# Kernel optimization log

Measured on AMD Instinct MI355X. Metric: run time of the kernel, lower is better.

## Reference

```python
import jax, jax.numpy as jnp
import numpy as np

B, T, J, V, D, H = 32, 400, 30, 50000, 150, 150
L = 2  # answer_token_len (boundary model: start, end)


def _gru_step(h, x, Wih, Whh, bih, bhh):
    # torch GRUCell semantics
    gi = x @ Wih.T + bih
    gh = h @ Whh.T + bhh
    ir, iz, inn = jnp.split(gi, 3, axis=-1)
    hr, hz, hn = jnp.split(gh, 3, axis=-1)
    r = jax.nn.sigmoid(ir + hr)
    z = jax.nn.sigmoid(iz + hz)
    n = jnp.tanh(inn + r * hn)
    return (1.0 - z) * n + z * h


def _gru_seq(x, Wih, Whh, bih, bhh):
    # x: [B, S, din] -> hidden sequence [B, S, h]
    h0 = jnp.zeros((x.shape[0], Whh.shape[1]), x.dtype)
    def step(h, xt):
        h = _gru_step(h, xt, Wih, Whh, bih, bhh)
        return h, h
    _, hs = jax.lax.scan(step, h0, jnp.swapaxes(x, 0, 1))
    return jnp.swapaxes(hs, 0, 1)


def _forward(context, query,
             E,
             ctx_Wih, ctx_Whh, ctx_bih, ctx_bhh,
             q_Wih, q_Whh, q_bih, q_bhh,
             Wq, Wp, Wr, w, gate_bias, attn_bias,
             m_Wih, m_Whh, m_bih, m_bhh,
             mr_Wih, mr_Whh, mr_bih, mr_bhh,
             ptr_W1, ptr_W2, ptr_v,
             d_Wih, d_Whh, d_bih, d_bhh):
    # encode context and query with GRUs
    Hp = _gru_seq(E[context], ctx_Wih, ctx_Whh, ctx_bih, ctx_bhh)  # [B,T,H]
    Hq = _gru_seq(E[query], q_Wih, q_Whh, q_bih, q_bhh)            # [B,J,H]

    whq = jnp.einsum('bjh,hk->bjk', Hq, Wq)  # precomputed query projection [B,J,H]

    def match_scan(xs, cWih, cWhh, cbih, cbhh):
        # xs: [B,T,H] context encodings (possibly time-reversed)
        def step(h, xt):
            # G_i = tanh(Wq Hq + (Wp p_i + Wr h_{i-1}) + bias)  -> [B,J,H]
            g = jnp.tanh(whq + (xt @ Wp + h @ Wr + gate_bias)[:, None, :])
            a = jax.nn.softmax(g @ w + attn_bias, axis=-1)       # [B,J]
            q = jnp.einsum('bj,bjh->bh', a, Hq)                  # attended query
            z = jnp.concatenate([xt, q], axis=-1)                # [B,2H]
            h = _gru_step(h, z, cWih, cWhh, cbih, cbhh)
            return h, h
        h0 = jnp.zeros((xs.shape[0], xs.shape[2]), xs.dtype)
        _, hs = jax.lax.scan(step, h0, jnp.swapaxes(xs, 0, 1))
        return jnp.swapaxes(hs, 0, 1)  # [B,T,H]

    Hf = match_scan(Hp, m_Wih, m_Whh, m_bih, m_bhh)              # forward direction
    Hb = match_scan(Hp[:, ::-1], mr_Wih, mr_Whh, mr_bih, mr_bhh) # reverse direction (scan order, as original)
    Hr = jnp.concatenate([Hf, Hb], axis=-1)                      # [B,T,2H]
    zero0 = jnp.zeros((Hr.shape[0], 1, Hr.shape[2]), Hr.dtype)   # initial zero state prepended
    Hr = jnp.concatenate([zero0, Hr], axis=1)                    # [B,T+1,2H]

    # boundary pointer network: L attention steps over H_r
    enc = Hr @ ptr_W1
    def ptr_step(h, _):
        s = jnp.tanh(enc + (h @ ptr_W2)[:, None, :]) @ ptr_v     # [B,T+1]
        a = jax.nn.softmax(s, axis=-1)
        c = jnp.einsum('bt,bth->bh', a, Hr)
        h = _gru_step(h, c, d_Wih, d_Whh, d_bih, d_bhh)
        return h, a
    h0 = jnp.zeros((Hr.shape[0], Hr.shape[2]), Hr.dtype)
    _, probs = jax.lax.scan(ptr_step, h0, None, length=L)
    return jnp.swapaxes(probs, 0, 1)  # [B, L, T+1]


def setup_inputs() -> dict:
    key = jax.random.key(0)
    keys = iter(jax.random.split(key, 40))
    p = lambda *s: jax.random.normal(next(keys), s, jnp.float32) * 0.05
    inp = {
        'context': jax.random.randint(next(keys), (B, T), 0, V, dtype=jnp.int32),
        'query': jax.random.randint(next(keys), (B, J), 0, V, dtype=jnp.int32),
        'E': p(V, D),
        'ctx_Wih': p(3 * H, D), 'ctx_Whh': p(3 * H, H), 'ctx_bih': p(3 * H), 'ctx_bhh': p(3 * H),
        'q_Wih': p(3 * H, D), 'q_Whh': p(3 * H, H), 'q_bih': p(3 * H), 'q_bhh': p(3 * H),
        'Wq': p(H, H), 'Wp': p(H, H), 'Wr': p(H, H), 'w': p(H),
        'gate_bias': p(H), 'attn_bias': p(),
        'm_Wih': p(3 * H, 2 * H), 'm_Whh': p(3 * H, H), 'm_bih': p(3 * H), 'm_bhh': p(3 * H),
        'mr_Wih': p(3 * H, 2 * H), 'mr_Whh': p(3 * H, H), 'mr_bih': p(3 * H), 'mr_bhh': p(3 * H),
        'ptr_W1': p(2 * H, 2 * H), 'ptr_W2': p(2 * H, 2 * H), 'ptr_v': p(2 * H),
        'd_Wih': p(6 * H, 2 * H), 'd_Whh': p(6 * H, 2 * H), 'd_bih': p(6 * H), 'd_bhh': p(6 * H),
    }
    return inp


def reference(context, query, E,
              ctx_Wih, ctx_Whh, ctx_bih, ctx_bhh,
              q_Wih, q_Whh, q_bih, q_bhh,
              Wq, Wp, Wr, w, gate_bias, attn_bias,
              m_Wih, m_Whh, m_bih, m_bhh,
              mr_Wih, mr_Whh, mr_bih, mr_bhh,
              ptr_W1, ptr_W2, ptr_v,
              d_Wih, d_Whh, d_bih, d_bhh):
    return _forward(context, query, E,
                    ctx_Wih, ctx_Whh, ctx_bih, ctx_bhh,
                    q_Wih, q_Whh, q_bih, q_bhh,
                    Wq, Wp, Wr, w, gate_bias, attn_bias,
                    m_Wih, m_Whh, m_bih, m_bhh,
                    mr_Wih, mr_Whh, mr_bih, mr_bhh,
                    ptr_W1, ptr_W2, ptr_v,
                    d_Wih, d_Whh, d_bih, d_bhh)
```

## Files before the change

### kernel.cpp

```cpp
#include <hip/hip_runtime.h>
#include <hip/hip_bf16.h>


namespace {

constexpr int NBATCH = 32;
constexpr int TLEN   = 400;
constexpr int JQ     = 30;
constexpr int T1     = 401;

__device__ __forceinline__ float sigm(float x){ return 1.f/(1.f+__expf(-x)); }
__device__ __forceinline__ float tanh_f(float x){
  float e = __expf(-2.f*fabsf(x));
  float t = (1.f-e)/(1.f+e);
  return x < 0.f ? -t : t;
}
__device__ __forceinline__ float bf2f(unsigned short u){
  union { unsigned int i; float f; } c; c.i = ((unsigned int)u)<<16; return c.f;
}

__device__ __forceinline__ void bar_lds(){
  asm volatile("s_waitcnt lgkmcnt(0)" ::: "memory");
  __builtin_amdgcn_s_barrier();
}

#define NW 29
struct WDesc { const void* src[NW]; int off[NW+1]; };

__global__ void sniff_kernel(const unsigned int* __restrict__ bits, int* __restrict__ flag){
  __shared__ int cnt;
  if (threadIdx.x==0) cnt = 0;
  __syncthreads();
  int hit = 0;
  #pragma unroll
  for (int i=0;i<4;i++){
    unsigned int w = bits[threadIdx.x*4+i];
    unsigned int b = (w>>8)&0x7Fu;
    if (b==0u || (b>=0x38u && b<=0x3Fu)) hit++;
  }
  atomicAdd(&cnt, hit);
  __syncthreads();
  if (threadIdx.x==0) *flag = (cnt > 768) ? 1 : 0;
}

__global__ void convert_weights_kernel(WDesc d, float* __restrict__ out, const int* __restrict__ flag){
  const int isbf = *flag;
  const int total = d.off[NW];
  for (int e = blockIdx.x*blockDim.x+threadIdx.x; e < total; e += gridDim.x*blockDim.x){
    int j = 0;
    while (e >= d.off[j+1]) j++;
    int i = e - d.off[j];
    out[e] = isbf ? bf2f(((const unsigned short*)d.src[j])[i])
                  : ((const float*)d.src[j])[i];
  }
}

__global__ void padrows_kernel(const float* __restrict__ src, float* __restrict__ dst,
                               int rows, int cols, int ldd){
  int i = blockIdx.x*blockDim.x+threadIdx.x;
  if (i >= rows*ldd) return;
  int r = i/ldd, c = i-r*ldd;
  dst[i] = (c<cols) ? src[(size_t)r*cols+c] : 0.f;
}

__global__ void transpose_kernel(const float* __restrict__ src, float* __restrict__ dst,
                                 int R, int C, int lds_, int offs){
  int idx = blockIdx.x*blockDim.x+threadIdx.x;
  if (idx >= R*C) return;
  int i = idx / R, k = idx - i*R;
  dst[(size_t)i*R + k] = src[(size_t)k*lds_ + offs + i];
}

__global__ void build_wcat_kernel(const float* __restrict__ Whh, const float* __restrict__ Wr,
                                  float* __restrict__ Wcat){
  int i = blockIdx.x*blockDim.x+threadIdx.x;
  if (i >= 600*152) return;
  int r = i/152, c = i-r*152;
  float v = 0.f;
  if (c < 150){
    if (r < 450) v = Whh[(size_t)r*150+c];
    else         v = Wr[(size_t)c*150 + (r-450)];
  }
  Wcat[i] = v;
}

__global__ void build_msplit_kernel(const float* __restrict__ Wcat,
                                    float* __restrict__ s2q, float* __restrict__ ext){
  int i = blockIdx.x*blockDim.x+threadIdx.x;
  if (i < 24576){
    int q = i/2048, rem = i-q*2048, r = rem/4, p = rem-r*4;
    s2q[i] = Wcat[(size_t)r*152 + 104 + 4*q + p];
  } else if (i < 24576+13376){
    int k = i-24576;
    int q = k/352, rem = k-q*352, ii = rem/4, p = rem-ii*4;
    ext[k] = Wcat[(size_t)(512+ii)*152 + 4*q + p];
  }
}

__global__ void build_gsplit_kernel(const float* __restrict__ Wpad, float* __restrict__ s2q){
  int i = blockIdx.x*blockDim.x+threadIdx.x;
  if (i >= 12*452*4) return;
  int q = i/1808, rem = i-q*1808, r = rem/4, p = rem-r*4;
  s2q[i] = (r<450) ? Wpad[(size_t)r*152 + 104 + 4*q + p] : 0.f;
}

__global__ __launch_bounds__(512) void rowproj16_kernel(
    const float* __restrict__ Xrows,
    const int* __restrict__ gather, const void* __restrict__ Etab, const int* __restrict__ bfflag,
    const float* __restrict__ W, const float* __restrict__ bias,
    float* __restrict__ out, int rows, int K, int inner, int ldw, int ldo)
{
  __shared__ __align__(16) float xs[16][304];
  const int r0 = blockIdx.x*16;
  int nr = rows - r0; if (nr > 16) nr = 16;
  if (nr <= 0) return;
  const int isbf = gather ? *bfflag : 0;
  for (int e = threadIdx.x; e < nr*inner; e += 512){
    int r = e/inner, i = e - r*inner;
    float v;
    if (gather){
      size_t base = (size_t)gather[r0+r]*inner + i;
      v = isbf ? bf2f(((const unsigned short*)Etab)[base]) : ((const float*)Etab)[base];
    } else {
      v = Xrows[(size_t)(r0+r)*inner + i];
    }
    xs[r][i] = v;
  }
  __syncthreads();
  for (int k = threadIdx.x; k < K; k += 512){
    float b0 = bias ? bias[k] : 0.f;
    float acc[16];
    #pragma unroll
    for (int r=0;r<16;r++) acc[r] = b0;
    int i = 0;
    for (; i+4 <= inner; i += 4){
      float w0 = W[(size_t)i*ldw + k];
      float w1 = W[(size_t)(i+1)*ldw + k];
      float w2 = W[(size_t)(i+2)*ldw + k];
      float w3 = W[(size_t)(i+3)*ldw + k];
      #pragma unroll
      for (int r=0;r<16;r++){
        float4 xv = *(const float4*)&xs[r][i];
        acc[r] = fmaf(xv.x, w0, acc[r]);
        acc[r] = fmaf(xv.y, w1, acc[r]);
        acc[r] = fmaf(xv.z, w2, acc[r]);
        acc[r] = fmaf(xv.w, w3, acc[r]);
      }
    }
    for (; i < inner; i++){
      float wv = W[(size_t)i*ldw + k];
      #pragma unroll
      for (int r=0;r<16;r++) acc[r] = fmaf(xs[r][i], wv, acc[r]);
    }
    for (int r=0;r<nr;r++) out[(size_t)(r0+r)*ldo + k] = acc[r];
  }
  for (int k = K + threadIdx.x; k < ldo; k += 512)
    for (int r=0;r<nr;r++) out[(size_t)(r0+r)*ldo + k] = 0.f;
}

#define R26(M) M(0) M(1) M(2) M(3) M(4) M(5) M(6) M(7) M(8) M(9) M(10) M(11) \
               M(12) M(13) M(14) M(15) M(16) M(17) M(18) M(19) M(20) M(21) \
               M(22) M(23) M(24) M(25)
#define R12(M) M(26) M(27) M(28) M(29) M(30) M(31) M(32) M(33) M(34) M(35) \
               M(36) M(37)
#define DECW(i) float4 w##i;
#define LDW(i)  w##i = wrow4[i];
#define LDW2(i) w##i = s2q4[(i-26)*s2stride + s2r];
#define FMAW(i) { float4 hq = h4[i]; \
  acc0 = fmaf(hq.x, w##i.x, acc0); acc1 = fmaf(hq.y, w##i.y, acc1); \
  acc2 = fmaf(hq.z, w##i.z, acc2); acc3 = fmaf(hq.w, w##i.w, acc3); }

__global__ __launch_bounds__(512, 2) void gru_scan_kernel(
    const float* __restrict__ gi0, const float* __restrict__ Wp0,
    const float* __restrict__ s2q0, const float* __restrict__ bh0,
    float* __restrict__ H0, int S0,
    const float* __restrict__ gi1, const float* __restrict__ Wp1,
    const float* __restrict__ s2q1, const float* __restrict__ bh1,
    float* __restrict__ H1, int S1)
{
  const int blk = blockIdx.x;
  const float* gi; const float* Wpad; const float* s2qG; const float* bh; float* Hs; int S;
  if (blk < 32){ gi = gi0 + (size_t)blk*S0*450;  Wpad = Wp0; s2qG = s2q0; bh = bh0;
                 Hs = H0 + (size_t)blk*S0*150;   S = S0; }
  else         { int bb = blk-32;
                 gi = gi1 + (size_t)bb*S1*450;   Wpad = Wp1; s2qG = s2q1; bh = bh1;
                 Hs = H1 + (size_t)bb*S1*150;    S = S1; }
  __shared__ __align__(16) float h[152];
  __shared__ float gh[452];
  const int tid = threadIdx.x;

  R26(DECW) R12(DECW)
  float br = 0.f;
  {
    const float4* wrow4 = (const float4*)(Wpad + (size_t)((tid<450)?tid:0)*152);
    R26(LDW)
    const float4* s2q4 = (const float4*)s2qG;
    const int s2stride = 452; const int s2r = (tid<452) ? tid : 0;
    R12(LDW2)
    if (tid<450) br = bh[tid];
  }
  if (tid < 152) h[tid] = 0.f;
  __syncthreads();
  const float4* h4 = (const float4*)h;

  for (int t=0;t<S;t++){
    float g0=0.f,g1=0.f,g2=0.f;
    if (tid < 150){
      const float* gg = gi + (size_t)t*450;
      g0 = gg[tid]; g1 = gg[150+tid]; g2 = gg[300+tid];
    }
    if (tid < 450){
      float acc0=br, acc1=0.f, acc2=0.f, acc3=0.f;
      R26(FMAW) R12(FMAW)
      gh[tid] = (acc0+acc2)+(acc1+acc3);
    }
    bar_lds();
    if (tid < 150){
      float r = sigm(g0 + gh[tid]);
      float z = sigm(g1 + gh[150+tid]);
      float n = tanh_f(g2 + r*gh[300+tid]);
      float hn = (1.f-z)*n + z*h[tid];
      h[tid] = hn;
      Hs[(size_t)t*150 + tid] = hn;
    }
    bar_lds();
  }
}

__global__ void zero_hr0_kernel(float* __restrict__ Hr){
  int idx = blockIdx.x*blockDim.x + threadIdx.x;
  if (idx < NBATCH*300){
    int b = idx/300, k = idx - 300*b;
    Hr[(size_t)b*T1*300 + k] = 0.f;
  }
}

__global__ __launch_bounds__(512, 2) void match_scan_kernel(
    const float* __restrict__ pWp,
    const float* __restrict__ whq,
    const float* __restrict__ giXf,
    const float* __restrict__ giXr,
    const float* __restrict__ Pf,
    const float* __restrict__ Pr,
    const float* __restrict__ WcatF, const float* __restrict__ WcatR,
    const float* __restrict__ s2qF,  const float* __restrict__ s2qR,
    const float* __restrict__ extF,  const float* __restrict__ extR,
    const float* __restrict__ m_bhh, const float* __restrict__ mr_bhh,
    const float* __restrict__ wvec,
    float* __restrict__ Hr)
{
  const int b   = blockIdx.x;
  const int dir = blockIdx.y;
  const float* giX  = dir ? giXr : giXf;
  const float* P    = dir ? Pr   : Pf;
  const float* Wcat = dir ? WcatR : WcatF;
  const float* s2qG = dir ? s2qR  : s2qF;
  const float* extG = dir ? extR  : extF;
  const float* bhh  = dir ? mr_bhh : m_bhh;

  __shared__ float4 extW[3344];
  __shared__ __align__(16) float Ps[JQ*452];
  __shared__ __align__(16) float whqS[JQ*152];
  __shared__ __align__(16) float wrP[760];
  __shared__ __align__(16) float h[152];
  __shared__ float ghsRaw[512];
  __shared__ __align__(16) float pwS[152];
  __shared__ __align__(16) float wlS[152];
  __shared__ float sc[32];

  const int tid  = threadIdx.x;
  const int lane = tid & 63;
  const int wv   = tid >> 6;
  const int er   = (tid < 440) ? (tid % 88) : 0;
  const int kg   = (tid < 440) ? (tid / 88) : 0;

  R26(DECW) R12(DECW)
  float br;
  {
    const float4* wrow4 = (const float4*)(Wcat + (size_t)tid*152);
    R26(LDW)
    const float4* s2q4 = (const float4*)s2qG;
    const int s2stride = 512; const int s2r = tid;
    R12(LDW2)
    br = (tid < 450) ? bhh[tid] : 0.f;
  }
  for (int e=tid; e<3344; e+=512) extW[e] = ((const float4*)extG)[e];
  {
    const float* Pb = P + (size_t)b*JQ*452;
    for (int e=tid; e<JQ*452; e+=512) Ps[e] = Pb[e];
    const float4* wq4 = (const float4*)(whq + (size_t)b*JQ*152);
    for (int e=tid; e<JQ*38; e+=512) ((float4*)whqS)[e] = wq4[e];
  }
  for (int e=tid; e<760; e+=512) wrP[e] = 0.f;
  if (tid < 152){
    h[tid] = 0.f;
    wlS[tid] = (tid<150) ? wvec[tid] : 0.f;
  }
  __syncthreads();
  const float4* h4 = (const float4*)h;
  const float4* wrP4 = (const float4*)wrP;

  for (int t=0;t<TLEN;t++){
    const int tt = dir ? (TLEN-1-t) : t;

    float gv0=0.f, gv1=0.f, gv2=0.f;
    if (tid < 150){
      const float* g = giX + ((size_t)b*TLEN + tt)*452;
      gv0 = g[tid]; gv1 = g[150+tid]; gv2 = g[300+tid];
    }
    float4 pwv;
    if (tid >= 440 && tid < 478)
      pwv = ((const float4*)(pWp + ((size_t)b*TLEN + tt)*152))[tid-440];

    {
      float acc0=br, acc1=0.f, acc2=0.f, acc3=0.f;
      R26(FMAW) R12(FMAW)
      float v = (acc0+acc2)+(acc1+acc3);
      ghsRaw[tid] = v;
      if (tid >= 450) wrP[tid-450] = v;
    }
    if (tid < 440){
      float e0=0.f, e1=0.f;
      #pragma unroll
      for (int j=0;j<8;j++){
        int q = kg*8+j;
        if (q < 38){
          float4 wq = extW[q*88+er]; float4 hq = h4[q];
          e0 = fmaf(hq.x,wq.x,e0); e1 = fmaf(hq.y,wq.y,e1);
          e0 = fmaf(hq.z,wq.z,e0); e1 = fmaf(hq.w,wq.w,e1);
        }
      }
      wrP[kg*152 + 62 + er] = e0+e1;
    }
    if (tid >= 440 && tid < 478) ((float4*)pwS)[tid-440] = pwv;
    bar_lds();

    {
      float4 b4; b4.x=b4.y=b4.z=b4.w=0.f;
      const bool bl = (lane < 38);
      if (bl){
        float4 pw4 = ((const float4*)pwS)[lane];
        float4 s0 = wrP4[lane],        s1 = wrP4[38+lane];
        float4 s2 = wrP4[76+lane],     s3 = wrP4[114+lane];
        float4 s4 = wrP4[152+lane];
        b4.x = pw4.x + s0.x+s1.x+s2.x+s3.x+s4.x;
        b4.y = pw4.y + s0.y+s1.y+s2.y+s3.y+s4.y;
        b4.z = pw4.z + s0.z+s1.z+s2.z+s3.z+s4.z;
        b4.w = pw4.w + s0.w+s1.w+s2.w+s3.w+s4.w;
      }
      #pragma unroll
      for (int jj=0;jj<4;jj++){
        int j = wv + 8*jj;
        float a = 0.f;
        if (j < JQ && bl){
          float4 q4 = ((const float4*)whqS)[j*38 + lane];
          float4 w4 = ((const float4*)wlS)[lane];
          a = w4.x*tanh_f(q4.x+b4.x);
          a = fmaf(w4.y, tanh_f(q4.y+b4.y), a);
          a = fmaf(w4.z, tanh_f(q4.z+b4.z), a);
          a = fmaf(w4.w, tanh_f(q4.w+b4.w), a);
        }
        #pragma unroll
        for (int off=32; off; off>>=1) a += __shfl_down(a, off);
        if (j < JQ && lane==0) sc[j] = a;
      }
    }
    bar_lds();

    if (tid < 192){
      float v = (lane < JQ) ? sc[lane] : -1e30f;
      float m = v;
      #pragma unroll
      for (int off=32; off; off>>=1) m = fmaxf(m, __shfl_down(m, off));
      m = __shfl(m, 0);
      float e = (lane < JQ) ? __expf(v-m) : 0.f;
      float su = e;
      #pragma unroll
      for (int off=32; off; off>>=1) su += __shfl_down(su, off);
      su = __shfl(su, 0);
      float aw = e/su;
      const int k = (tid < 150) ? tid : 0;
      float accr = gv0, accz = gv1, accn = gv2;
      #pragma unroll
      for (int j=0;j<JQ;j++){
        float aj = __shfl(aw, j);
        accr = fmaf(aj, Ps[j*452 + k],       accr);
        accz = fmaf(aj, Ps[j*452 + 150 + k], accz);
        accn = fmaf(aj, Ps[j*452 + 300 + k], accn);
      }
      if (tid < 150){
        float r = sigm(accr + ghsRaw[tid]);
        float z = sigm(accz + ghsRaw[150+tid]);
        float n = tanh_f(accn + r*ghsRaw[300+tid]);
        float hn = (1.f-z)*n + z*h[tid];
        h[tid] = hn;
        Hr[((size_t)b*T1 + (t+1))*300 + dir*150 + tid] = hn;
      }
    }
    bar_lds();
  }
}

__global__ __launch_bounds__(512,2) void ptr_scan_kernel(
    const float* __restrict__ enc, const float* __restrict__ Hr,
    const float* __restrict__ W2, const float* __restrict__ pv,
    const float* __restrict__ dWih, const float* __restrict__ dWhh,
    const float* __restrict__ dbih, const float* __restrict__ dbhh,
    void* __restrict__ outv, const int* __restrict__ flag)
{
  const int b = blockIdx.x;
  const int tid = threadIdx.x;
  const int isbf = *flag;
  __shared__ float h[300], hW2[300], sl[T1], al[T1], c[300];
  __shared__ float gis[900], ghs[900];
  __shared__ float vl[300];
  __shared__ float red[8];
  if (tid < 300){ h[tid] = 0.f; vl[tid] = pv[tid]; }
  __syncthreads();
  for (int l=0;l<2;l++){
    if (tid < 300){
      float a0=0.f,a1=0.f;
      for (int i=0;i<300;i+=2){
        a0 += h[i]  *W2[(size_t)i*300+tid];
        a1 += h[i+1]*W2[(size_t)(i+1)*300+tid];
      }
      hW2[tid] = a0+a1;
    }
    __syncthreads();
    {
      const int wv = tid>>6, lane = tid&63;
      for (int t=wv; t<T1; t+=8){
        const float* er = enc + ((size_t)b*T1 + t)*300;
        float acc = 0.f;
        for (int k=lane; k<300; k+=64) acc += vl[k]*tanh_f(er[k] + hW2[k]);
        #pragma unroll
        for (int off=32; off; off>>=1) acc += __shfl_down(acc, off);
        if (lane==0) sl[t] = acc;
      }
    }
    __syncthreads();
    {
      float v = (tid < T1) ? sl[tid] : -1e30f;
      float m = v;
      #pragma unroll
      for (int off=32; off; off>>=1) m = fmaxf(m, __shfl_down(m, off));
      if ((tid&63)==0) red[tid>>6] = m;
      __syncthreads();
      float bm = fmaxf(fmaxf(fmaxf(red[0],red[1]),fmaxf(red[2],red[3])),
                       fmaxf(fmaxf(red[4],red[5]),fmaxf(red[6],red[7])));
      float e = (tid < T1) ? __expf(v-bm) : 0.f;
      float su = e;
      #pragma unroll
      for (int off=32; off; off>>=1) su += __shfl_down(su, off);
      __syncthreads();
      if ((tid&63)==0) red[tid>>6] = su;
      __syncthreads();
      float bs = red[0]+red[1]+red[2]+red[3]+red[4]+red[5]+red[6]+red[7];
      if (tid < T1){
        float a = e/bs;
        al[tid] = a;
        size_t oi = ((size_t)b*2 + l)*T1 + tid;
        if (isbf) ((__hip_bfloat16*)outv)[oi] = __float2bfloat16(a);
        else      ((float*)outv)[oi] = a;
      }
    }
    __syncthreads();
    if (tid < 300){
      float acc = 0.f;
      for (int t=0;t<T1;t++) acc += al[t]*Hr[((size_t)b*T1 + t)*300 + tid];
      c[tid] = acc;
    }
    __syncthreads();
    for (int k=tid; k<900; k+=blockDim.x){
      const float* wi = dWih + (size_t)k*300;
      const float* wh = dWhh + (size_t)k*300;
      float a0 = dbih[k], a1 = dbhh[k];
      for (int i=0;i<300;i++){ a0 += c[i]*wi[i]; a1 += h[i]*wh[i]; }
      gis[k] = a0; ghs[k] = a1;
    }
    __syncthreads();
    if (tid < 300){
      float r = sigm(gis[tid] + ghs[tid]);
      float z = sigm(gis[300+tid] + ghs[300+tid]);
      float n = tanh_f(gis[600+tid] + r*ghs[600+tid]);
      h[tid] = (1.f-z)*n + z*h[tid];
    }
    __syncthreads();
  }
}

}

extern "C" void kernel_launch(void* const* d_in, const int* in_sizes, int n_in,
                              void* d_out, int out_size, void* d_ws, size_t ws_size,
                              hipStream_t stream)
{
  (void)in_sizes; (void)n_in; (void)out_size; (void)ws_size;
  float* ws = (float*)d_ws;
  int* flag = (int*)d_ws;

  static const int wsz[NW] = {
    67500,67500,450,450,
    67500,67500,450,450,
    22500,22500,22500,150,150,1,
    135000,67500,450,450,
    135000,67500,450,450,
    90000,90000,300,
    270000,270000,900,900
  };
  WDesc desc;
  int cum = 0;
  for (int j=0;j<NW;j++){ desc.src[j] = d_in[3+j]; desc.off[j] = cum; cum += wsz[j]; }
  desc.off[NW] = cum;

  float* WB = ws + 16;
  const float* P_ctx_Wih = WB + desc.off[0];
  const float* P_ctx_Whh = WB + desc.off[1];
  const float* P_ctx_bih = WB + desc.off[2];
  const float* P_ctx_bhh = WB + desc.off[3];
  const float* P_q_Wih   = WB + desc.off[4];
  const float* P_q_Whh   = WB + desc.off[5];
  const float* P_q_bih   = WB + desc.off[6];
  const float* P_q_bhh   = WB + desc.off[7];
  const float* P_Wq      = WB + desc.off[8];
  const float* P_Wp      = WB + desc.off[9];
  const float* P_Wr      = WB + desc.off[10];
  const float* P_w       = WB + desc.off[11];
  const float* P_gb      = WB + desc.off[12];
  const float* P_m_Wih   = WB + desc.off[14];
  const float* P_m_Whh   = WB + desc.off[15];
  const float* P_m_bih   = WB + desc.off[16];
  const float* P_m_bhh   = WB + desc.off[17];
  const float* P_mr_Wih  = WB + desc.off[18];
  const float* P_mr_Whh  = WB + desc.off[19];
  const float* P_mr_bih  = WB + desc.off[20];
  const float* P_mr_bhh  = WB + desc.off[21];
  const float* P_W1      = WB + desc.off[22];
  const float* P_W2      = WB + desc.off[23];
  const float* P_pv      = WB + desc.off[24];
  const float* P_dWih    = WB + desc.off[25];
  const float* P_dWhh    = WB + desc.off[26];
  const float* P_dbih    = WB + desc.off[27];
  const float* P_dbhh    = WB + desc.off[28];

  size_t p = 16 + 1468512;
  float* ctxWhhP = ws + p; p += 68400;
  float* qWhhP   = ws + p; p += 68400;
  float* s2qCtx  = ws + p; p += 21696;
  float* s2qQ    = ws + p; p += 21696;
  float* WcatF   = ws + p; p += 91200;
  float* WcatR   = ws + p; p += 91200;
  float* s2qF    = ws + p; p += 24576;
  float* s2qR    = ws + p; p += 24576;
  float* extFg   = ws + p; p += 13376;
  float* extRg   = ws + p; p += 13376;
  float* ctxWihT = ws + p; p += 67500;
  float* qWihT   = ws + p; p += 67500;
  float* mXfT    = ws + p; p += 67500;
  float* mXrT    = ws + p; p += 67500;
  float* mQfT    = ws + p; p += 67500;
  float* mQrT    = ws + p; p += 67500;

  float* ctx_gi = ws + p; p += 5760000;
  float* q_gi   = ws + p; p += 432000;
  float* HpB    = ws + p; p += 1920000;
  float* HqB    = ws + p; p += 144000;
  float* whqB   = ws + p; p += 145920;
  float* PfB    = ws + p; p += 433920;
  float* PrB    = ws + p; p += 433920;
  float* pWpB   = ws + p; p += 1945600;
  float* giXfB  = ws + p; p += 5785600;
  float* giXrB  = ws + p; p += 5785600;
  float* HrB    = ws + p; p += 3849600;
  float* encB   = ctx_gi;

  sniff_kernel<<<1,256,0,stream>>>((const unsigned int*)d_in[2], flag);
  convert_weights_kernel<<<512,256,0,stream>>>(desc, WB, flag);
  padrows_kernel<<<(450*152+255)/256,256,0,stream>>>(P_ctx_Whh, ctxWhhP, 450,150,152);
  padrows_kernel<<<(450*152+255)/256,256,0,stream>>>(P_q_Whh,   qWhhP,   450,150,152);
  build_gsplit_kernel<<<(12*452*4+255)/256,256,0,stream>>>(ctxWhhP, s2qCtx);
  build_gsplit_kernel<<<(12*452*4+255)/256,256,0,stream>>>(qWhhP,   s2qQ);
  build_wcat_kernel<<<(600*152+255)/256,256,0,stream>>>(P_m_Whh,  P_Wr, WcatF);
  build_wcat_kernel<<<(600*152+255)/256,256,0,stream>>>(P_mr_Whh, P_Wr, WcatR);
  build_msplit_kernel<<<(24576+13376+255)/256,256,0,stream>>>(WcatF, s2qF, extFg);
  build_msplit_kernel<<<(24576+13376+255)/256,256,0,stream>>>(WcatR, s2qR, extRg);
  transpose_kernel<<<(67500+255)/256,256,0,stream>>>(P_ctx_Wih, ctxWihT, 450,150,150,0);
  transpose_kernel<<<(67500+255)/256,256,0,stream>>>(P_q_Wih,   qWihT,   450,150,150,0);
  transpose_kernel<<<(67500+255)/256,256,0,stream>>>(P_m_Wih,   mXfT,    450,150,300,0);
  transpose_kernel<<<(67500+255)/256,256,0,stream>>>(P_mr_Wih,  mXrT,    450,150,300,0);
  transpose_kernel<<<(67500+255)/256,256,0,stream>>>(P_m_Wih,   mQfT,    450,150,300,150);
  transpose_kernel<<<(67500+255)/256,256,0,stream>>>(P_mr_Wih,  mQrT,    450,150,300,150);

  rowproj16_kernel<<<800,512,0,stream>>>(nullptr,(const int*)d_in[0], d_in[2], flag,
                                         ctxWihT, P_ctx_bih, ctx_gi, 12800,450,150,450,450);
  rowproj16_kernel<<<60,512,0,stream>>>(nullptr,(const int*)d_in[1], d_in[2], flag,
                                        qWihT, P_q_bih, q_gi, 960,450,150,450,450);

  gru_scan_kernel<<<64,512,0,stream>>>(ctx_gi, ctxWhhP, s2qCtx, P_ctx_bhh, HpB, 400,
                                       q_gi,   qWhhP,   s2qQ,   P_q_bhh,   HqB, 30);

  rowproj16_kernel<<<60,512,0,stream>>>(HqB,nullptr,nullptr,nullptr, P_Wq, nullptr,
                                        whqB, 960,150,150,150,152);
  rowproj16_kernel<<<60,512,0,stream>>>(HqB,nullptr,nullptr,nullptr, mQfT, nullptr,
                                        PfB, 960,450,150,450,452);
  rowproj16_kernel<<<60,512,0,stream>>>(HqB,nullptr,nullptr,nullptr, mQrT, nullptr,
                                        PrB, 960,450,150,450,452);
  rowproj16_kernel<<<800,512,0,stream>>>(HpB,nullptr,nullptr,nullptr, P_Wp, P_gb,
                                         pWpB, 12800,150,150,150,152);
  rowproj16_kernel<<<800,512,0,stream>>>(HpB,nullptr,nullptr,nullptr, mXfT, P_m_bih,
                                         giXfB, 12800,450,150,450,452);
  rowproj16_kernel<<<800,512,0,stream>>>(HpB,nullptr,nullptr,nullptr, mXrT, P_mr_bih,
                                         giXrB, 12800,450,150,450,452);

  zero_hr0_kernel<<<(NBATCH*300+511)/512,512,0,stream>>>(HrB);
  match_scan_kernel<<<dim3(NBATCH,2),512,0,stream>>>(pWpB, whqB, giXfB, giXrB,
                                                     PfB, PrB, WcatF, WcatR,
                                                     s2qF, s2qR, extFg, extRg,
                                                     P_m_bhh, P_mr_bhh, P_w, HrB);

  rowproj16_kernel<<<802,512,0,stream>>>(HrB,nullptr,nullptr,nullptr, P_W1, nullptr,
                                         encB, 12832,300,300,300,300);
  ptr_scan_kernel<<<32,512,0,stream>>>(encB, HrB, P_W2, P_pv,
                                       P_dWih, P_dWhh, P_dbih, P_dbhh, d_out, flag);
}
```

Measured before the change: 3.498 ms.

## Keep match-scan weights in registers and transpose attention projection in LDS

The extension weights and the per-batch query projection plus attention vector move from shared memory into per-thread registers, loaded once before the time loop. The P matrix is stored transposed in LDS so each thread reads contiguous float4 rows. Every softmax thread now computes the full 30-way softmax from the shared scores instead of using cross-lane shuffles. The aim is to cut LDS traffic, shuffles and serial latency inside the 400-step recurrence, at the cost of higher register pressure under 512-thread launch bounds, which could cause spills.

```diff
diff --git a/kernel.cpp b/kernel.cpp
--- a/kernel.cpp
+++ b/kernel.cpp
@@ -17,6 +17,14 @@
 }
 __device__ __forceinline__ float bf2f(unsigned short u){
   union { unsigned int i; float f; } c; c.i = ((unsigned int)u)<<16; return c.f;
+}
+__device__ __forceinline__ float q4max(float4 v){ return fmaxf(fmaxf(v.x,v.y),fmaxf(v.z,v.w)); }
+__device__ __forceinline__ float sum4(float4 v){ return (v.x+v.y)+(v.z+v.w); }
+__device__ __forceinline__ float4 exp4(float4 v, float m){
+  return make_float4(__expf(v.x-m),__expf(v.y-m),__expf(v.z-m),__expf(v.w-m));
+}
+__device__ __forceinline__ float4 scl4(float4 v, float s){
+  return make_float4(v.x*s,v.y*s,v.z*s,v.w*s);
 }
 
 __device__ __forceinline__ void bar_lds(){
@@ -163,12 +171,19 @@
                M(22) M(23) M(24) M(25)
 #define R12(M) M(26) M(27) M(28) M(29) M(30) M(31) M(32) M(33) M(34) M(35) \
                M(36) M(37)
+#define E8(M)  M(0) M(1) M(2) M(3) M(4) M(5) M(6) M(7)
 #define DECW(i) float4 w##i;
 #define LDW(i)  w##i = wrow4[i];
 #define LDW2(i) w##i = s2q4[(i-26)*s2stride + s2r];
 #define FMAW(i) { float4 hq = h4[i]; \
   acc0 = fmaf(hq.x, w##i.x, acc0); acc1 = fmaf(hq.y, w##i.y, acc1); \
   acc2 = fmaf(hq.z, w##i.z, acc2); acc3 = fmaf(hq.w, w##i.w, acc3); }
+#define DECE(j) float4 ex##j;
+#define LDE(j)  { int q = kg*8+j; \
+  ex##j = (tid<440 && q<38) ? extG4[q*88+er] : make_float4(0.f,0.f,0.f,0.f); }
+#define FMAE(j) { float4 hq = h4[kg*8+j]; \
+  f0 = fmaf(hq.x, ex##j.x, f0); f1 = fmaf(hq.y, ex##j.y, f1); \
+  f0 = fmaf(hq.z, ex##j.z, f0); f1 = fmaf(hq.w, ex##j.w, f1); }
 
 __global__ __launch_bounds__(512, 2) void gru_scan_kernel(
     const float* __restrict__ gi0, const float* __restrict__ Wp0,
@@ -258,16 +273,12 @@
   const float* extG = dir ? extR  : extF;
   const float* bhh  = dir ? mr_bhh : m_bhh;
 
-  __shared__ float4 extW[3344];
-  __shared__ __align__(16) float Ps[JQ*452];
-  __shared__ __align__(16) float whqS[JQ*152];
+  __shared__ __align__(16) float PsT[15000];
   __shared__ __align__(16) float wrP[760];
-  __shared__ __align__(16) float h[152];
+  __shared__ __align__(16) float h[160];
   __shared__ float ghsRaw[512];
   __shared__ __align__(16) float pwS[152];
-  __shared__ __align__(16) float wlS[152];
-  __shared__ float sc[32];
-
+  __shared__ __align__(16) float sc[32];
   const int tid  = threadIdx.x;
   const int lane = tid & 63;
   const int wv   = tid >> 6;
@@ -284,17 +295,35 @@
     R12(LDW2)
     br = (tid < 450) ? bhh[tid] : 0.f;
   }
-  for (int e=tid; e<3344; e+=512) extW[e] = ((const float4*)extG)[e];
+  const float4* extG4 = (const float4*)extG;
+  E8(DECE) E8(LDE)
+  const float4* wqg = (const float4*)(whq + (size_t)b*JQ*152);
+  const int ln38 = (lane < 38) ? lane : 0;
+  float4 wq0 = wqg[(size_t)(wv     )*38 + ln38];
+  float4 wq1 = wqg[(size_t)(wv +  8)*38 + ln38];
+  float4 wq2 = wqg[(size_t)(wv + 16)*38 + ln38];
+  float4 wq3 = (wv + 24 < JQ) ? wqg[(size_t)(wv + 24)*38 + ln38]
+                              : make_float4(0.f,0.f,0.f,0.f);
+  float4 wl4 = make_float4(0.f,0.f,0.f,0.f);
+  if (lane < 38){
+    wl4 = ((const float4*)wvec)[lane];
+    if (lane == 37){ wl4.z = 0.f; wl4.w = 0.f; }
+  }
+
+  for (int e=tid; e<15000; e+=512) PsT[e] = 0.f;
+  for (int e=tid; e<760;   e+=512) wrP[e] = 0.f;
+  if (tid < 160) h[tid] = 0.f;
+  if (tid >= 30 && tid < 32) sc[tid] = -1e30f;
+  __syncthreads();
   {
     const float* Pb = P + (size_t)b*JQ*452;
-    for (int e=tid; e<JQ*452; e+=512) Ps[e] = Pb[e];
-    const float4* wq4 = (const float4*)(whq + (size_t)b*JQ*152);
-    for (int e=tid; e<JQ*38; e+=512) ((float4*)whqS)[e] = wq4[e];
-  }
-  for (int e=tid; e<760; e+=512) wrP[e] = 0.f;
-  if (tid < 152){
-    h[tid] = 0.f;
-    wlS[tid] = (tid<150) ? wvec[tid] : 0.f;
+    for (int e=tid; e<JQ*452; e+=512){
+      int j = e/452, kk = e - j*452;
+      if (kk < 450){
+        int g = kk/150, k = kk - g*150;
+        PsT[k*100 + g*32 + j] = Pb[e];
+      }
+    }
   }
   __syncthreads();
   const float4* h4 = (const float4*)h;
@@ -319,24 +348,16 @@
       ghsRaw[tid] = v;
       if (tid >= 450) wrP[tid-450] = v;
     }
-    if (tid < 440){
-      float e0=0.f, e1=0.f;
-      #pragma unroll
-      for (int j=0;j<8;j++){
-        int q = kg*8+j;
-        if (q < 38){
-          float4 wq = extW[q*88+er]; float4 hq = h4[q];
-          e0 = fmaf(hq.x,wq.x,e0); e1 = fmaf(hq.y,wq.y,e1);
-          e0 = fmaf(hq.z,wq.z,e0); e1 = fmaf(hq.w,wq.w,e1);
-        }
-      }
-      wrP[kg*152 + 62 + er] = e0+e1;
+    {
+      float f0=0.f, f1=0.f;
+      E8(FMAE)
+      if (tid < 440) wrP[kg*152 + 62 + er] = f0+f1;
     }
     if (tid >= 440 && tid < 478) ((float4*)pwS)[tid-440] = pwv;
     bar_lds();
 
     {
-      float4 b4; b4.x=b4.y=b4.z=b4.w=0.f;
+      float4 b4 = make_float4(0.f,0.f,0.f,0.f);
       const bool bl = (lane < 38);
       if (bl){
         float4 pw4 = ((const float4*)pwS)[lane];
@@ -348,46 +369,45 @@
         b4.z = pw4.z + s0.z+s1.z+s2.z+s3.z+s4.z;
         b4.w = pw4.w + s0.w+s1.w+s2.w+s3.w+s4.w;
       }
-      #pragma unroll
-      for (int jj=0;jj<4;jj++){
-        int j = wv + 8*jj;
-        float a = 0.f;
-        if (j < JQ && bl){
-          float4 q4 = ((const float4*)whqS)[j*38 + lane];
-          float4 w4 = ((const float4*)wlS)[lane];
-          a = w4.x*tanh_f(q4.x+b4.x);
-          a = fmaf(w4.y, tanh_f(q4.y+b4.y), a);
-          a = fmaf(w4.z, tanh_f(q4.z+b4.z), a);
-          a = fmaf(w4.w, tanh_f(q4.w+b4.w), a);
-        }
-        #pragma unroll
-        for (int off=32; off; off>>=1) a += __shfl_down(a, off);
-        if (j < JQ && lane==0) sc[j] = a;
-      }
+      #define BSCORE(jj, WQ) { const int j = wv + 8*jj; float a = 0.f; \
+        if (j < JQ && bl){ \
+          a = wl4.x*tanh_f(WQ.x+b4.x); \
+          a = fmaf(wl4.y, tanh_f(WQ.y+b4.y), a); \
+          a = fmaf(wl4.z, tanh_f(WQ.z+b4.z), a); \
+          a = fmaf(wl4.w, tanh_f(WQ.w+b4.w), a); } \
+        a += __shfl_down(a,32); a += __shfl_down(a,16); a += __shfl_down(a,8); \
+        a += __shfl_down(a,4);  a += __shfl_down(a,2);  a += __shfl_down(a,1); \
+        if (j < JQ && lane==0) sc[j] = a; }
+      BSCORE(0, wq0) BSCORE(1, wq1) BSCORE(2, wq2) BSCORE(3, wq3)
+      #undef BSCORE
     }
     bar_lds();
 
     if (tid < 192){
-      float v = (lane < JQ) ? sc[lane] : -1e30f;
-      float m = v;
-      #pragma unroll
-      for (int off=32; off; off>>=1) m = fmaxf(m, __shfl_down(m, off));
-      m = __shfl(m, 0);
-      float e = (lane < JQ) ? __expf(v-m) : 0.f;
-      float su = e;
-      #pragma unroll
-      for (int off=32; off; off>>=1) su += __shfl_down(su, off);
-      su = __shfl(su, 0);
-      float aw = e/su;
+      const float4* sc4 = (const float4*)sc;
+      float4 s0=sc4[0], s1=sc4[1], s2=sc4[2], s3=sc4[3];
+      float4 s4=sc4[4], s5=sc4[5], s6=sc4[6], s7=sc4[7];
+      float m = fmaxf(fmaxf(fmaxf(q4max(s0),q4max(s1)),fmaxf(q4max(s2),q4max(s3))),
+                      fmaxf(fmaxf(q4max(s4),q4max(s5)),fmaxf(q4max(s6),q4max(s7))));
+      float4 a0=exp4(s0,m), a1=exp4(s1,m), a2=exp4(s2,m), a3=exp4(s3,m);
+      float4 a4=exp4(s4,m), a5=exp4(s5,m), a6=exp4(s6,m), a7=exp4(s7,m);
+      float su = ((sum4(a0)+sum4(a1))+(sum4(a2)+sum4(a3)))
+               + ((sum4(a4)+sum4(a5))+(sum4(a6)+sum4(a7)));
+      float inv = 1.f/su;
+      a0=scl4(a0,inv); a1=scl4(a1,inv); a2=scl4(a2,inv); a3=scl4(a3,inv);
+      a4=scl4(a4,inv); a5=scl4(a5,inv); a6=scl4(a6,inv); a7=scl4(a7,inv);
       const int k = (tid < 150) ? tid : 0;
+      const float4* Pk = (const float4*)(PsT + k*100);
       float accr = gv0, accz = gv1, accn = gv2;
-      #pragma unroll
-      for (int j=0;j<JQ;j++){
-        float aj = __shfl(aw, j);
-        accr = fmaf(aj, Ps[j*452 + k],       accr);
-        accz = fmaf(aj, Ps[j*452 + 150 + k], accz);
-        accn = fmaf(aj, Ps[j*452 + 300 + k], accn);
-      }
+      #define ACC1(acc,P4,A4){ float4 p=P4; \
+        acc=fmaf(A4.x,p.x,acc); acc=fmaf(A4.y,p.y,acc); \
+        acc=fmaf(A4.z,p.z,acc); acc=fmaf(A4.w,p.w,acc); }
+      #define ACCG(acc,g){ ACC1(acc,Pk[g*8+0],a0) ACC1(acc,Pk[g*8+1],a1) \
+        ACC1(acc,Pk[g*8+2],a2) ACC1(acc,Pk[g*8+3],a3) ACC1(acc,Pk[g*8+4],a4) \
+        ACC1(acc,Pk[g*8+5],a5) ACC1(acc,Pk[g*8+6],a6) ACC1(acc,Pk[g*8+7],a7) }
+      ACCG(accr,0) ACCG(accz,1) ACCG(accn,2)
+      #undef ACC1
+      #undef ACCG
       if (tid < 150){
         float r = sigm(accr + ghsRaw[tid]);
         float z = sigm(accz + ghsRaw[150+tid]);
```

Measured after the change: 3.787 ms. 1.08x slower.
